# Kernel optimization log

Measured on AMD Instinct MI355X. Metric: run time of the kernel, lower is better.

The kernel has to match this reference:

```python
import jax, jax.numpy as jnp
import numpy as np

DIM = 1024
HEADS = 16
HEAD_DIM = DIM // HEADS
B, S = 2, 2048


def setup_inputs() -> dict:
    key = jax.random.key(0)
    ks = jax.random.split(key, 12)
    scale = 1.0 / np.sqrt(DIM)
    inp = {
        "Q_in": jax.random.normal(ks[0], (B, S, DIM), jnp.float32),
        "K_in": jax.random.normal(ks[1], (B, S, DIM), jnp.float32),
        "V_in": jax.random.normal(ks[2], (B, S, DIM), jnp.float32),
        "Wq": jax.random.normal(ks[3], (DIM, DIM), jnp.float32) * scale,
        "bq": jnp.zeros((DIM,), jnp.float32),
        "Wk": jax.random.normal(ks[4], (DIM, DIM), jnp.float32) * scale,
        "bk": jnp.zeros((DIM,), jnp.float32),
        "Wv": jax.random.normal(ks[5], (DIM, DIM), jnp.float32) * scale,
        "bv": jnp.zeros((DIM,), jnp.float32),
        "Wo": jax.random.normal(ks[6], (DIM, DIM), jnp.float32) * scale,
        "bo": jnp.zeros((DIM,), jnp.float32),
        "is_causal": 1,
    }
    return inp


def reference(Q_in, K_in, V_in, Wq, bq, Wk, bk, Wv, bv, Wo, bo, is_causal):
    b, s, d = Q_in.shape
    hd = d // HEADS
    # linear projections (torch nn.Linear: x @ W.T + b), split heads -> [b,h,s,hd]
    Q = (Q_in @ Wq.T + bq).reshape(b, s, HEADS, hd).transpose(0, 2, 1, 3)
    K = (K_in @ Wk.T + bk).reshape(b, s, HEADS, hd).transpose(0, 2, 1, 3)
    V = (V_in @ Wv.T + bv).reshape(b, s, HEADS, hd).transpose(0, 2, 1, 3)
    # full [b,h,s,s] score matrix, as in the original (no fused SDPA)
    scores = jnp.einsum("bhqd,bhkd->bhqk", Q, K) / jnp.sqrt(jnp.float32(hd))
    if is_causal:
        causal = jnp.tril(jnp.ones((s, s), dtype=bool))  # [s,s]
        scores = jnp.where(causal, scores, jnp.float32(-jnp.inf))
    attn = jax.nn.softmax(scores, axis=-1)
    # dropout is identity (eval mode) for a deterministic reference
    out = jnp.einsum("bhqk,bhkd->bhqd", attn, V)
    out = out.transpose(0, 2, 1, 3).reshape(b, s, d)
    return out @ Wo.T + bo
```

## Files before the change

kernel.cpp:

```cpp
#include <hip/hip_runtime.h>
#include <hip/hip_bf16.h>
#include <stdint.h>

#define HEADS 16
#define HD 64
#define BATCH 2
#define SEQ 2048
#define NDIM 1024
#define MROWS (BATCH * SEQ)

typedef __attribute__((ext_vector_type(8))) __bf16 bf16x8;
typedef __attribute__((ext_vector_type(4))) __bf16 bf16x4;
typedef __attribute__((ext_vector_type(4))) float f32x4;

#define LOG2E 1.4426950408889634f
#define SOFTMAX_C 16.0f

#if __has_builtin(__builtin_amdgcn_exp2f)
#define EXP2(x) __builtin_amdgcn_exp2f(x)
#else
#define EXP2(x) exp2f(x)
#endif

#define GLDS16(g, l)                                                          \
  __builtin_amdgcn_global_load_lds(                                           \
      (const __attribute__((address_space(1))) unsigned int*)(g),             \
      (__attribute__((address_space(3))) unsigned int*)(l), 16, 0, 0)

__global__ void cvt_w_kernel(const float* __restrict__ wq, const float* __restrict__ wk,
                             const float* __restrict__ wv, const float* __restrict__ wo,
                             __bf16* __restrict__ owq, __bf16* __restrict__ owk,
                             __bf16* __restrict__ owv, __bf16* __restrict__ owo) {
  const int id = blockIdx.x;
  const int m = id >> 10;
  const int blk = id & 1023;
  const float* in = (m == 0) ? wq : (m == 1) ? wk : (m == 2) ? wv : wo;
  __bf16* out = (m == 0) ? owq : (m == 1) ? owk : (m == 2) ? owv : owo;
  const size_t i = ((size_t)blk * 256 + threadIdx.x) * 4;
  const float4 v = *(const float4*)(in + i);
  bf16x4 o = {(__bf16)v.x, (__bf16)v.y, (__bf16)v.z, (__bf16)v.w};
  *(bf16x4*)(out + i) = o;
}

template <int BNF, bool TRC, bool AF32>
__device__ __forceinline__ void gemm_core(const void* __restrict__ Araw,
                                          const __bf16* __restrict__ B,
                                          int m0, int n0,
                                          char* lA, char* lB,
                                          f32x4 acc[4][BNF]) {
  constexpr int BBUF = BNF * 2048;
  const int t = threadIdx.x;
  const int lane = t & 63;
  const int llo = lane & 15, lhi = lane >> 4;
  const int wid = t >> 6;
  const int wrow = (wid >> 1) * 64;
  const int wcol = (wid & 1) * (BNF * 16);

  const int sl = (t & 7) ^ ((t >> 3) & 7);
  const int srg = 2 * (t >> 3) + (sl >> 2);
  const int cg = (sl & 3) * 8;

  const __bf16* pB0 = B + (size_t)(n0 + srg) * 1024 + cg;
  const __bf16* pB1 = B + (size_t)(n0 + (BNF == 4 ? 64 : 0) + srg) * 1024 + cg;

#pragma unroll
  for (int mf = 0; mf < 4; ++mf)
#pragma unroll
    for (int nf = 0; nf < BNF; ++nf)
      acc[mf][nf] = (f32x4){0.f, 0.f, 0.f, 0.f};

  const int fcol = ((((llo & 1) << 2) | lhi) ^ (llo >> 1)) << 4;

#define DSREAD_MFMA                                                           \
  do {                                                                        \
    bf16x8 af[4], bfr[BNF];                                                   \
    _Pragma("unroll")                                                         \
    for (int mf = 0; mf < 4; ++mf) {                                          \
      const int R = wrow + mf * 16 + llo;                                     \
      af[mf] = *(const bf16x8*)(lA + cb * 8192 + (R >> 1) * 128 + fcol);      \
    }                                                                         \
    _Pragma("unroll")                                                         \
    for (int nf = 0; nf < BNF; ++nf) {                                        \
      const int R = wcol + nf * 16 + llo;                                     \
      bfr[nf] = *(const bf16x8*)(lB + cb * BBUF + (R >> 1) * 128 + fcol);     \
    }                                                                         \
    __builtin_amdgcn_s_setprio(1);                                            \
    _Pragma("unroll")                                                         \
    for (int mf = 0; mf < 4; ++mf)                                            \
      _Pragma("unroll")                                                       \
      for (int nf = 0; nf < BNF; ++nf)                                        \
        acc[mf][nf] = TRC                                                     \
            ? __builtin_amdgcn_mfma_f32_16x16x32_bf16(bfr[nf], af[mf],        \
                                                      acc[mf][nf], 0, 0, 0)   \
            : __builtin_amdgcn_mfma_f32_16x16x32_bf16(af[mf], bfr[nf],        \
                                                      acc[mf][nf], 0, 0, 0);  \
    __builtin_amdgcn_s_setprio(0);                                            \
  } while (0)

  if constexpr (!AF32) {
    const __bf16* A = (const __bf16*)Araw;
    constexpr int NLD = (BNF == 4) ? 4 : 3;
    const __bf16* pA0 = A + (size_t)(m0 + srg) * 1024 + cg;
    const __bf16* pA1 = A + (size_t)(m0 + 64 + srg) * 1024 + cg;

#define STAGE_G(buf, k0)                                                      \
  do {                                                                        \
    GLDS16(pA0 + (k0), lA + (buf) * 8192 + t * 16);                           \
    GLDS16(pA1 + (k0), lA + (buf) * 8192 + 4096 + t * 16);                    \
    GLDS16(pB0 + (k0), lB + (buf) * BBUF + t * 16);                           \
    if (BNF == 4) GLDS16(pB1 + (k0), lB + (buf) * BBUF + 4096 + t * 16);      \
  } while (0)

    STAGE_G(0, 0);
    STAGE_G(1, 32);

    int cb = 0;
    for (int k0 = 0; k0 < 1024; k0 += 32) {
      const int step = k0 >> 5;
      if (step + 2 < 32) {
        const int sb = (cb >= 1) ? (cb - 1) : (cb + 2);
        STAGE_G(sb, k0 + 64);
        asm volatile("s_waitcnt vmcnt(%0)" :: "i"(2 * NLD) : "memory");
      } else if (step + 1 < 32) {
        asm volatile("s_waitcnt vmcnt(%0)" :: "i"(NLD) : "memory");
      } else {
        asm volatile("s_waitcnt vmcnt(0)" ::: "memory");
      }
      __builtin_amdgcn_s_barrier();
      __builtin_amdgcn_sched_barrier(0);
      DSREAD_MFMA;
      __builtin_amdgcn_s_barrier();
      cb = (cb == 2) ? 0 : (cb + 1);
    }
#undef STAGE_G
  } else {
    const float* fA = (const float*)Araw;
    const float* fpA0 = fA + (size_t)(m0 + srg) * 1024 + cg;
    const float* fpA1 = fA + (size_t)(m0 + 64 + srg) * 1024 + cg;

#define STAGEB(buf, k0)                                                       \
  do {                                                                        \
    GLDS16(pB0 + (k0), lB + (buf) * BBUF + t * 16);                           \
    if (BNF == 4) GLDS16(pB1 + (k0), lB + (buf) * BBUF + 4096 + t * 16);      \
  } while (0)

#define WRITEA(buf, sa, sb_, sc, sd)                                          \
  do {                                                                        \
    bf16x8 v0, v1;                                                            \
    v0[0]=(__bf16)(sa).x; v0[1]=(__bf16)(sa).y; v0[2]=(__bf16)(sa).z; v0[3]=(__bf16)(sa).w; \
    v0[4]=(__bf16)(sb_).x; v0[5]=(__bf16)(sb_).y; v0[6]=(__bf16)(sb_).z; v0[7]=(__bf16)(sb_).w; \
    v1[0]=(__bf16)(sc).x; v1[1]=(__bf16)(sc).y; v1[2]=(__bf16)(sc).z; v1[3]=(__bf16)(sc).w; \
    v1[4]=(__bf16)(sd).x; v1[5]=(__bf16)(sd).y; v1[6]=(__bf16)(sd).z; v1[7]=(__bf16)(sd).w; \
    *(bf16x8*)(lA + (buf) * 8192 + t * 16) = v0;                              \
    *(bf16x8*)(lA + (buf) * 8192 + 4096 + t * 16) = v1;                       \
  } while (0)

    float4 p0a, p0b, p0c, p0d;
    float4 p1a, p1b, p1c, p1d;

    p0a = *(const float4*)(fpA0 + 0);  p0b = *(const float4*)(fpA0 + 4);
    p0c = *(const float4*)(fpA1 + 0);  p0d = *(const float4*)(fpA1 + 4);
    WRITEA(0, p0a, p0b, p0c, p0d);
    STAGEB(0, 0);
    STAGEB(1, 32);
    p1a = *(const float4*)(fpA0 + 32); p1b = *(const float4*)(fpA0 + 36);
    p1c = *(const float4*)(fpA1 + 32); p1d = *(const float4*)(fpA1 + 36);

    int cb = 0;

#define QSTEP(K0CUR, LA_, LB_, LC_, LD_, WA_, WB_, WC_, WD_)                  \
  {                                                                           \
    const int step_ = (K0CUR) >> 5;                                           \
    const int wb_ = (cb == 2) ? 0 : cb + 1;                                   \
    const int sb_ = (wb_ == 2) ? 0 : wb_ + 1;                                 \
    if (step_ + 2 < 32) {                                                     \
      STAGEB(sb_, (K0CUR) + 64);                                              \
      LA_ = *(const float4*)(fpA0 + (K0CUR) + 64);                            \
      LB_ = *(const float4*)(fpA0 + (K0CUR) + 68);                            \
      LC_ = *(const float4*)(fpA1 + (K0CUR) + 64);                            \
      LD_ = *(const float4*)(fpA1 + (K0CUR) + 68);                            \
    }                                                                         \
    if (step_ + 1 < 32) WRITEA(wb_, WA_, WB_, WC_, WD_);                      \
    if (step_ + 2 < 32) {                                                     \
      asm volatile("s_waitcnt vmcnt(6)" ::: "memory");                        \
    } else {                                                                  \
      asm volatile("s_waitcnt vmcnt(0)" ::: "memory");                        \
    }                                                                         \
    asm volatile("s_waitcnt lgkmcnt(0)" ::: "memory");                        \
    __builtin_amdgcn_s_barrier();                                             \
    __builtin_amdgcn_sched_barrier(0);                                        \
    DSREAD_MFMA;                                                              \
    __builtin_amdgcn_s_barrier();                                             \
    cb = (cb == 2) ? 0 : (cb + 1);                                            \
  }

    for (int k0 = 0; k0 < 1024; k0 += 64) {
      QSTEP(k0,      p0a, p0b, p0c, p0d,  p1a, p1b, p1c, p1d);
      QSTEP(k0 + 32, p1a, p1b, p1c, p1d,  p0a, p0b, p0c, p0d);
    }
#undef QSTEP
#undef WRITEA
#undef STAGEB
  }
#undef DSREAD_MFMA
}

__global__ __launch_bounds__(256, 3)
void qkv_gemm_kernel(const float* __restrict__ Xq, const float* __restrict__ Xk,
                     const float* __restrict__ Xv, const __bf16* __restrict__ Wq,
                     const __bf16* __restrict__ Wk, const __bf16* __restrict__ Wv,
                     const float* __restrict__ bq, const float* __restrict__ bk,
                     const float* __restrict__ bv, __bf16* __restrict__ Qh,
                     __bf16* __restrict__ Kh, __bf16* __restrict__ Vt) {
  __shared__ __align__(16) char ldsA[3 * 8192];
  __shared__ __align__(16) char ldsB[3 * 8192];

  const int lid = blockIdx.x;
  const int xcd = lid & 7, slot = lid >> 3;
  const int y = slot >> 2;
  const int m0 = (xcd * 4 + (slot & 3)) * 128;
  const int mat = y >> 3;
  const int n0 = (y & 7) * 128;

  const void* A = (mat == 0) ? (const void*)Xq
                 : (mat == 1) ? (const void*)Xk : (const void*)Xv;
  const __bf16* B = (mat == 0) ? Wq : (mat == 1) ? Wk : Wv;
  const float* bias = (mat == 0) ? bq : (mat == 1) ? bk : bv;

  const int t = threadIdx.x;
  const int lane = t & 63;
  const int llo = lane & 15, lhi = lane >> 4;
  const int wid = t >> 6;
  const int wrow = (wid >> 1) * 64;
  const int wcol = (wid & 1) * 64;

  f32x4 acc[4][4];
  if (mat < 2) {
    gemm_core<4, true, true>(A, B, m0, n0, ldsA, ldsB, acc);
    __bf16* dst = (mat == 0) ? Qh : Kh;
    const float qs = (mat == 0) ? (0.125f * LOG2E) : 1.0f;
#pragma unroll
    for (int nf = 0; nf < 4; ++nf) {
      const int cbase = n0 + wcol + nf * 16 + lhi * 4;
      const float4 b4 = *(const float4*)(bias + cbase);
      const int h = cbase >> 6, d0 = cbase & 63;
#pragma unroll
      for (int mf = 0; mf < 4; ++mf) {
        const int sg = m0 + wrow + mf * 16 + llo;
        const int b = sg >> 11, s0 = sg & 2047;
        bf16x4 pk;
        pk[0] = (__bf16)((acc[mf][nf][0] + b4.x) * qs);
        pk[1] = (__bf16)((acc[mf][nf][1] + b4.y) * qs);
        pk[2] = (__bf16)((acc[mf][nf][2] + b4.z) * qs);
        pk[3] = (__bf16)((acc[mf][nf][3] + b4.w) * qs);
        *(bf16x4*)(dst + ((size_t)(b * HEADS + h) * SEQ + s0) * HD + d0) = pk;
      }
    }
  } else {
    gemm_core<4, false, true>(A, B, m0, n0, ldsA, ldsB, acc);
#pragma unroll
    for (int nf = 0; nf < 4; ++nf) {
      const int cfull = n0 + wcol + nf * 16 + llo;
      const int h = cfull >> 6, d = cfull & 63;
      const float bb = bias[cfull];
#pragma unroll
      for (int mf = 0; mf < 4; ++mf) {
        const int row0 = m0 + wrow + mf * 16 + lhi * 4;
        const int b = row0 >> 11;
        const int s0 = row0 & 2047;
        bf16x4 pk;
#pragma unroll
        for (int j = 0; j < 4; ++j) pk[j] = (__bf16)(acc[mf][nf][j] + bb);
        *(bf16x4*)(Vt + ((size_t)(b * HEADS + h) * HD + d) * SEQ + s0) = pk;
      }
    }
  }
}

__global__ __launch_bounds__(256, 4)
void attn_kernel(const __bf16* __restrict__ Qh, const __bf16* __restrict__ Kh,
                 const __bf16* __restrict__ Vt, __bf16* __restrict__ O,
                 const int* __restrict__ causal_flag) {
  __shared__ __align__(16) __bf16 kbuf[2][64 * 64];
  __shared__ __align__(16) __bf16 vbuf[2][64 * 64];
  __shared__ __align__(16) __bf16 pbuf[4][16 * 64];

  const int t = threadIdx.x;
  const int lane = t & 63;
  const int llo = lane & 15, lhi = lane >> 4;
  const int w = t >> 6;
  const int causal = causal_flag[0];

  const int lid = blockIdx.x;
  const int xcd = lid & 7, slot = lid >> 3;
  const int group = slot >> 5, r = slot & 31;
  const int bh = xcd + 8 * group;
  const int b = bh >> 4, h = bh & 15;
  const int rr = (group >= 2) ? ((r + 8) & 31) : r;
  const int qt = (group & 1) ? (31 - rr) : rr;

  const __bf16* Qb = Qh + (size_t)bh * SEQ * HD;
  const __bf16* Kb = Kh + (size_t)bh * SEQ * HD;
  const __bf16* Vb = Vt + (size_t)bh * HD * SEQ;

  const int sr = t >> 3;
  const int sce = (((t & 7) * 16) ^ ((sr & 7) << 4)) >> 1;
  const int swz = (llo & 7) << 4;

  char* const pw = (char*)&pbuf[w][0];

  const int qw = qt * 64 + w * 16;
  const int nt = causal ? (qt + 1) : (SEQ / 64);

  bf16x8 bQ[2];
#pragma unroll
  for (int ks = 0; ks < 2; ++ks)
    bQ[ks] = *(const bf16x8*)(Qb + (size_t)(qw + llo) * HD + ks * 32 + lhi * 8);

  float lrun = 0.f;
  f32x4 accO[4];
#pragma unroll
  for (int nf = 0; nf < 4; ++nf) accO[nf] = (f32x4){0.f, 0.f, 0.f, 0.f};

  GLDS16(Kb + (size_t)sr * HD + sce,        (char*)&kbuf[0][0] + t * 16);
  GLDS16(Kb + (size_t)(32 + sr) * HD + sce, (char*)&kbuf[0][0] + 4096 + t * 16);
  GLDS16(Vb + (size_t)sr * SEQ + sce,       (char*)&vbuf[0][0] + t * 16);
  GLDS16(Vb + (size_t)(32 + sr) * SEQ + sce,(char*)&vbuf[0][0] + 4096 + t * 16);
  __syncthreads();
  int cur = 0;

  for (int tkv = 0; tkv < nt; ++tkv) {
    if (tkv + 1 < nt) {
      const int k0s = (tkv + 1) * 64;
      char* kd = (char*)&kbuf[cur ^ 1][0];
      char* vd = (char*)&vbuf[cur ^ 1][0];
      GLDS16(Kb + (size_t)(k0s + sr) * HD + sce,        kd + t * 16);
      GLDS16(Kb + (size_t)(k0s + 32 + sr) * HD + sce,   kd + 4096 + t * 16);
      GLDS16(Vb + (size_t)sr * SEQ + k0s + sce,         vd + t * 16);
      GLDS16(Vb + (size_t)(32 + sr) * SEQ + k0s + sce,  vd + 4096 + t * 16);
    }
    const int k0 = tkv * 64;
    const char* kb = (const char*)&kbuf[cur][0];
    const char* vb = (const char*)&vbuf[cur][0];

    f32x4 s[4];
#pragma unroll
    for (int nf = 0; nf < 4; ++nf) s[nf] = (f32x4){0.f, 0.f, 0.f, 0.f};
    __builtin_amdgcn_s_setprio(1);
#pragma unroll
    for (int ks = 0; ks < 2; ++ks)
#pragma unroll
      for (int nf = 0; nf < 4; ++nf) {
        bf16x8 aK = *(const bf16x8*)(kb + (nf * 16 + llo) * 128 +
                                     ((ks * 64 + lhi * 16) ^ swz));
        s[nf] = __builtin_amdgcn_mfma_f32_16x16x32_bf16(aK, bQ[ks], s[nf], 0, 0, 0);
      }
    __builtin_amdgcn_s_setprio(0);

    if (causal && tkv == qt) {
      const int qrow = qw + llo;
#pragma unroll
      for (int nf = 0; nf < 4; ++nf)
#pragma unroll
        for (int j = 0; j < 4; ++j)
          if (k0 + nf * 16 + lhi * 4 + j > qrow) s[nf][j] = -1e30f;
    }

#pragma unroll
    for (int nf = 0; nf < 4; ++nf)
#pragma unroll
      for (int j = 0; j < 4; ++j) {
        const float pv = EXP2(s[nf][j] - SOFTMAX_C);
        s[nf][j] = pv;
        lrun += pv;
      }

#pragma unroll
    for (int nf = 0; nf < 4; ++nf) {
      bf16x4 pk = {(__bf16)s[nf][0], (__bf16)s[nf][1], (__bf16)s[nf][2],
                   (__bf16)s[nf][3]};
      *(bf16x4*)(pw + llo * 128 + ((32 * nf + 8 * lhi) ^ swz)) = pk;
    }
    __builtin_amdgcn_s_setprio(1);
#pragma unroll
    for (int ks2 = 0; ks2 < 2; ++ks2) {
      bf16x8 bP = *(const bf16x8*)(pw + llo * 128 + ((64 * ks2 + 16 * lhi) ^ swz));
#pragma unroll
      for (int nf = 0; nf < 4; ++nf) {
        bf16x8 aV = *(const bf16x8*)(vb + (nf * 16 + llo) * 128 +
                                     ((64 * ks2 + 16 * lhi) ^ swz));
        accO[nf] = __builtin_amdgcn_mfma_f32_16x16x32_bf16(aV, bP, accO[nf], 0, 0, 0);
      }
    }
    __builtin_amdgcn_s_setprio(0);
    __syncthreads();
    cur ^= 1;
  }

  lrun += __shfl_xor(lrun, 16, 64);
  lrun += __shfl_xor(lrun, 32, 64);
  const float linv = 1.f / lrun;
  const int srow = qw + llo;
#pragma unroll
  for (int nf = 0; nf < 4; ++nf) {
    bf16x4 pk;
#pragma unroll
    for (int j = 0; j < 4; ++j) pk[j] = (__bf16)(accO[nf][j] * linv);
    *(bf16x4*)(O + ((size_t)(b * SEQ + srow) * HEADS + h) * HD + nf * 16 +
               lhi * 4) = pk;
  }
}

__global__ __launch_bounds__(256, 4)
void out_gemm_kernel(const __bf16* __restrict__ Oin, const __bf16* __restrict__ Wo,
                     const float* __restrict__ bo, float* __restrict__ out) {
  __shared__ __align__(16) char ldsA[3 * 8192];
  __shared__ __align__(16) char ldsB[3 * 4096];

  const int lid = blockIdx.x;
  const int xcd = lid & 7, slot = lid >> 3;
  const int n0 = (slot >> 2) * 64;
  const int m0 = (xcd * 4 + (slot & 3)) * 128;

  f32x4 acc[4][2];
  gemm_core<2, false, false>((const void*)Oin, Wo, m0, n0, ldsA, ldsB, acc);

  const int t = threadIdx.x;
  const int lane = t & 63;
  const int llo = lane & 15, lhi = lane >> 4;
  const int wid = t >> 6;
  const int wrow = (wid >> 1) * 64;
  const int wcol = (wid & 1) * 32;

#pragma unroll
  for (int nf = 0; nf < 2; ++nf) {
    const int col = n0 + wcol + nf * 16 + llo;
    const float bb = bo[col];
#pragma unroll
    for (int mf = 0; mf < 4; ++mf)
#pragma unroll
      for (int j = 0; j < 4; ++j) {
        const int row = m0 + wrow + mf * 16 + lhi * 4 + j;
        out[(size_t)row * NDIM + col] = acc[mf][nf][j] + bb;
      }
  }
}

extern "C" void kernel_launch(void* const* d_in, const int* in_sizes, int n_in,
                              void* d_out, int out_size, void* d_ws, size_t ws_size,
                              hipStream_t stream) {
  const float* Q_in = (const float*)d_in[0];
  const float* K_in = (const float*)d_in[1];
  const float* V_in = (const float*)d_in[2];
  const float* Wq = (const float*)d_in[3];
  const float* bq = (const float*)d_in[4];
  const float* Wk = (const float*)d_in[5];
  const float* bk = (const float*)d_in[6];
  const float* Wv = (const float*)d_in[7];
  const float* bv = (const float*)d_in[8];
  const float* Wo = (const float*)d_in[9];
  const float* bo = (const float*)d_in[10];
  const int* causal = (const int*)d_in[11];
  float* out = (float*)d_out;

  char* p = (char*)d_ws;
  const size_t SZ_X = (size_t)MROWS * NDIM * 2;
  const size_t SZ_W = (size_t)NDIM * NDIM * 2;
  __bf16* bWq = (__bf16*)p; p += SZ_W;
  __bf16* bWk = (__bf16*)p; p += SZ_W;
  __bf16* bWv = (__bf16*)p; p += SZ_W;
  __bf16* bWo = (__bf16*)p; p += SZ_W;
  __bf16* Qh  = (__bf16*)p; p += SZ_X;
  __bf16* Kh  = (__bf16*)p; p += SZ_X;
  __bf16* Vt  = (__bf16*)p; p += SZ_X;
  __bf16* Obf = (__bf16*)p; p += SZ_X;

  cvt_w_kernel<<<4096, 256, 0, stream>>>(Wq, Wk, Wv, Wo, bWq, bWk, bWv, bWo);

  qkv_gemm_kernel<<<768, 256, 0, stream>>>(Q_in, K_in, V_in, bWq, bWk, bWv,
                                           bq, bk, bv, Qh, Kh, Vt);
  attn_kernel<<<1024, 256, 0, stream>>>(Qh, Kh, Vt, Obf, causal);
  out_gemm_kernel<<<512, 256, 0, stream>>>(Obf, bWo, bo, out);
}
```

Baseline: 107.4 us.

## Deepen A-operand register prefetch to three stages in QKV GEMM

Result: no change. 108.1 us (+0.7%).

```diff
diff --git a/kernel.cpp b/kernel.cpp
--- a/kernel.cpp
+++ b/kernel.cpp
@@ -155,34 +155,41 @@
     *(bf16x8*)(lA + (buf) * 8192 + 4096 + t * 16) = v1;                       \
   } while (0)
 
-    float4 p0a, p0b, p0c, p0d;
-    float4 p1a, p1b, p1c, p1d;
-
-    p0a = *(const float4*)(fpA0 + 0);  p0b = *(const float4*)(fpA0 + 4);
-    p0c = *(const float4*)(fpA1 + 0);  p0d = *(const float4*)(fpA1 + 4);
-    WRITEA(0, p0a, p0b, p0c, p0d);
+    float4 a0x, a0y, a0z, a0w;
+    float4 a1x, a1y, a1z, a1w;
+    float4 a2x, a2y, a2z, a2w;
+
     STAGEB(0, 0);
     STAGEB(1, 32);
-    p1a = *(const float4*)(fpA0 + 32); p1b = *(const float4*)(fpA0 + 36);
-    p1c = *(const float4*)(fpA1 + 32); p1d = *(const float4*)(fpA1 + 36);
+    a0x = *(const float4*)(fpA0 + 0);  a0y = *(const float4*)(fpA0 + 4);
+    a0z = *(const float4*)(fpA1 + 0);  a0w = *(const float4*)(fpA1 + 4);
+    a1x = *(const float4*)(fpA0 + 32); a1y = *(const float4*)(fpA0 + 36);
+    a1z = *(const float4*)(fpA1 + 32); a1w = *(const float4*)(fpA1 + 36);
+    a2x = *(const float4*)(fpA0 + 64); a2y = *(const float4*)(fpA0 + 68);
+    a2z = *(const float4*)(fpA1 + 64); a2w = *(const float4*)(fpA1 + 68);
+    WRITEA(0, a0x, a0y, a0z, a0w);
 
     int cb = 0;
 
-#define QSTEP(K0CUR, LA_, LB_, LC_, LD_, WA_, WB_, WC_, WD_)                  \
+#define QSTEP(K0CUR, L0, L1, L2, L3, W0, W1, W2, W3)                          \
   {                                                                           \
     const int step_ = (K0CUR) >> 5;                                           \
     const int wb_ = (cb == 2) ? 0 : cb + 1;                                   \
-    const int sb_ = (wb_ == 2) ? 0 : wb_ + 1;                                 \
-    if (step_ + 2 < 32) {                                                     \
-      STAGEB(sb_, (K0CUR) + 64);                                              \
-      LA_ = *(const float4*)(fpA0 + (K0CUR) + 64);                            \
-      LB_ = *(const float4*)(fpA0 + (K0CUR) + 68);                            \
-      LC_ = *(const float4*)(fpA1 + (K0CUR) + 64);                            \
-      LD_ = *(const float4*)(fpA1 + (K0CUR) + 68);                            \
+    const int sb_ = (cb == 0) ? 2 : cb - 1;                     \
+    if (step_ + 2 < 32) STAGEB(sb_, (K0CUR) + 64);                            \
+    if (step_ + 3 < 32) {                                                     \
+      L0 = *(const float4*)(fpA0 + (K0CUR) + 96);                             \
+      L1 = *(const float4*)(fpA0 + (K0CUR) + 100);                            \
+      L2 = *(const float4*)(fpA1 + (K0CUR) + 96);                             \
+      L3 = *(const float4*)(fpA1 + (K0CUR) + 100);                            \
     }                                                                         \
-    if (step_ + 1 < 32) WRITEA(wb_, WA_, WB_, WC_, WD_);                      \
-    if (step_ + 2 < 32) {                                                     \
-      asm volatile("s_waitcnt vmcnt(6)" ::: "memory");                        \
+    if (step_ + 1 < 32) WRITEA(wb_, W0, W1, W2, W3);                          \
+    if (step_ <= 28) {                                                        \
+      asm volatile("s_waitcnt vmcnt(12)" ::: "memory");                       \
+    } else if (step_ == 29) {                                                 \
+      asm volatile("s_waitcnt vmcnt(8)" ::: "memory");                        \
+    } else if (step_ == 30) {                                                 \
+      asm volatile("s_waitcnt vmcnt(2)" ::: "memory");                        \
     } else {                                                                  \
       asm volatile("s_waitcnt vmcnt(0)" ::: "memory");                        \
     }                                                                         \
@@ -194,9 +201,12 @@
     cb = (cb == 2) ? 0 : (cb + 1);                                            \
   }
 
-    for (int k0 = 0; k0 < 1024; k0 += 64) {
-      QSTEP(k0,      p0a, p0b, p0c, p0d,  p1a, p1b, p1c, p1d);
-      QSTEP(k0 + 32, p1a, p1b, p1c, p1d,  p0a, p0b, p0c, p0d);
+    for (int k0 = 0; k0 < 1024; k0 += 96) {
+      QSTEP(k0,      a0x, a0y, a0z, a0w,  a1x, a1y, a1z, a1w);
+      if (k0 + 32 < 1024)
+        QSTEP(k0 + 32, a1x, a1y, a1z, a1w,  a2x, a2y, a2z, a2w);
+      if (k0 + 64 < 1024)
+        QSTEP(k0 + 64, a2x, a2y, a2z, a2w,  a0x, a0y, a0z, a0w);
     }
 #undef QSTEP
 #undef WRITEA
```
